# Kernel optimization log

Hardware: AMD Instinct MI355X
Metric: run time of the kernel (lower is better)

The kernel has to match this reference:

```python
import jax, jax.numpy as jnp
import numpy as np

WINDOW = 512
GLOBAL = 64
NEG = -1e9


def setup_inputs() -> dict:
    key = jax.random.key(0)
    kq, kk, kv = jax.random.split(key, 3)
    B, H, S, D = 2, 16, 4096, 64
    q = jax.random.normal(kq, (B, H, S, D), dtype=jnp.float32)
    k = jax.random.normal(kk, (B, H, S, D), dtype=jnp.float32)
    v = jax.random.normal(kv, (B, H, S, D), dtype=jnp.float32)
    return {"q": q, "k": k, "v": v}


def _swa(q, k, v):
    # Causal sliding-window attention (window WINDOW, inclusive of self)
    # with the first GLOBAL queries attending to ALL keys (non-causal),
    # matching the torch reference's per-position SDPA loop.
    B, H, S, D = q.shape
    W, G = WINDOW, GLOBAL
    nb = S // W  # seq chosen as multiple of window
    scale = jnp.asarray(1.0 / np.sqrt(D), q.dtype)

    # --- banded (sliding-window) part, computed blockwise ---
    qb = q.reshape(B, H, nb, W, D)
    # pad one window of zeros in front so each query block sees blocks [b-1, b]
    kp = jnp.pad(k, ((0, 0), (0, 0), (W, 0), (0, 0))).reshape(B, H, nb + 1, W, D)
    vp = jnp.pad(v, ((0, 0), (0, 0), (W, 0), (0, 0))).reshape(B, H, nb + 1, W, D)
    kc = jnp.concatenate([kp[:, :, :nb], kp[:, :, 1:]], axis=3)  # (B,H,nb,2W,D)
    vc = jnp.concatenate([vp[:, :, :nb], vp[:, :, 1:]], axis=3)  # (B,H,nb,2W,D)

    scores = jnp.einsum("bhnqd,bhnkd->bhnqk", qb, kc) * scale  # (B,H,nb,W,2W)

    # query global pos i = b*W + r; key global pos j = (b-1)*W + c, c in [0,2W)
    # window constraint i-W+1 <= j <= i  <=>  r+1 <= c <= r+W
    r = jnp.arange(W)[:, None]
    c = jnp.arange(2 * W)[None, :]
    band = (c >= r + 1) & (c <= r + W)              # (W, 2W)
    first = band & (c >= W)                          # block 0: j >= 0
    blk0 = (jnp.arange(nb) == 0)[:, None, None]
    mask = jnp.where(blk0, first[None], band[None])  # (nb, W, 2W)

    scores = jnp.where(mask[None, None], scores, jnp.asarray(NEG, scores.dtype))
    probs = jax.nn.softmax(scores, axis=-1)
    out = jnp.einsum("bhnqk,bhnkd->bhnqd", probs, vc).reshape(B, H, S, D)

    # --- global prefix: first G queries attend to all keys ---
    sg = jnp.einsum("bhqd,bhkd->bhqk", q[:, :, :G], k) * scale  # (B,H,G,S)
    og = jnp.einsum("bhqk,bhkd->bhqd", jax.nn.softmax(sg, axis=-1), v)
    return out.at[:, :, :G].set(og)


def reference(q, k, v):
    return _swa(q, k, v)
```

## Files before the change

kernel.cpp:

```cpp
#include <hip/hip_runtime.h>


typedef __attribute__((ext_vector_type(4))) float  f32x4;
typedef __attribute__((ext_vector_type(8))) short  s16x8;

#define S_LEN  4096
#define D_HEAD 64
#define SCALE_L2 (0.125f * 1.44269504088896340736f)
#define MINIT  (-1e5f)
#define MASKV  (-1e30f)

static __device__ __forceinline__ short f2bf(float x) {
  unsigned u = __builtin_bit_cast(unsigned, x);
  return (short)((u + 0x8000u) >> 16);
}

static __device__ __forceinline__ f32x4 mfma32(s16x8 a, s16x8 b, f32x4 c) {
  return __builtin_amdgcn_mfma_f32_16x16x32_bf16(a, b, c, 0, 0, 0);
}

extern "C" __global__ void __launch_bounds__(256, 4)
swa_fused_kernel(const float* __restrict__ qg, const float* __restrict__ kg,
                 const float* __restrict__ vg, float* __restrict__ outg) {
  __shared__ __align__(16) char LDSBUF[32768];
  __shared__ float MLB[4][2][16];

  const int tid = threadIdx.x;
  const int w   = tid >> 6;
  const int l   = tid & 63;
  const int g   = l >> 4;
  const int ql  = l & 15;
  const int bi  = blockIdx.x;

  if (bi < 128) {
    const int bh = bi >> 2, qsub = bi & 3;
    const float* Q = qg + (size_t)bh * S_LEN * D_HEAD;
    const float* K = kg + (size_t)bh * S_LEN * D_HEAD;
    const float* V = vg + (size_t)bh * S_LEN * D_HEAD;
    float* O = outg + (size_t)bh * S_LEN * D_HEAD;
    const int qrow = qsub * 16 + ql;

    s16x8 qf[2];
#pragma unroll
    for (int h = 0; h < 2; ++h) {
      const float* p = Q + qrow * 64 + h * 32 + g * 8;
      f32x4 a = *(const f32x4*)p, b = *(const f32x4*)(p + 4);
      s16x8 r;
#pragma unroll
      for (int e = 0; e < 4; ++e) { r[e] = f2bf(a[e] * SCALE_L2); r[4 + e] = f2bf(b[e] * SCALE_L2); }
      qf[h] = r;
    }

    short* kfw = (short*)(LDSBUF + w * 8192);
    short* vfw = (short*)(LDSBUF + w * 8192 + 4096);

    f32x4 acc[4] = {{0,0,0,0},{0,0,0,0},{0,0,0,0},{0,0,0,0}};
    float m = MINIT, lsum = 0.f;

    for (int it = 0; it < 32; ++it) {
      const int k0 = w * 1024 + it * 32;
#pragma unroll
      for (int fb = 0; fb < 4; ++fb) {
        int row = k0 + ((fb >> 1) << 4) + ql;
        int d0  = ((fb & 1) << 5) + (g << 3);
        const float* p = K + row * 64 + d0;
        f32x4 a = *(const f32x4*)p, b = *(const f32x4*)(p + 4);
        s16x8 r;
#pragma unroll
        for (int e = 0; e < 4; ++e) { r[e] = f2bf(a[e]); r[4 + e] = f2bf(b[e]); }
        *(s16x8*)(kfw + (fb * 64 + l) * 8) = r;
      }
#pragma unroll
      for (int fb = 0; fb < 4; ++fb) {
        int dd = fb * 16 + ql;
        int kk = k0 + (g << 2);
        const float* p = V + kk * 64 + dd;
        s16x8 r;
#pragma unroll
        for (int j = 0; j < 4; ++j) { r[j] = f2bf(p[j * 64]); r[4 + j] = f2bf(p[(16 + j) * 64]); }
        *(s16x8*)(vfw + (fb * 64 + l) * 8) = r;
      }
      f32x4 c[2];
#pragma unroll
      for (int kt = 0; kt < 2; ++kt) {
        s16x8 a0 = *(const s16x8*)(kfw + ((kt * 2 + 0) * 64 + l) * 8);
        s16x8 a1 = *(const s16x8*)(kfw + ((kt * 2 + 1) * 64 + l) * 8);
        f32x4 cc = {0,0,0,0};
        cc = mfma32(a0, qf[0], cc);
        cc = mfma32(a1, qf[1], cc);
        c[kt] = cc;
      }
      float rm = MASKV;
#pragma unroll
      for (int kt = 0; kt < 2; ++kt)
#pragma unroll
        for (int r = 0; r < 4; ++r) rm = fmaxf(rm, c[kt][r]);
      rm = fmaxf(rm, __shfl_xor(rm, 16));
      rm = fmaxf(rm, __shfl_xor(rm, 32));
      float mn = fmaxf(m, rm);
      float al = __builtin_amdgcn_exp2f(m - mn);
      float rs = 0.f;
      float pv[2][4];
#pragma unroll
      for (int kt = 0; kt < 2; ++kt)
#pragma unroll
        for (int r = 0; r < 4; ++r) { float e2 = __builtin_amdgcn_exp2f(c[kt][r] - mn); pv[kt][r] = e2; rs += e2; }
      rs += __shfl_xor(rs, 16);
      rs += __shfl_xor(rs, 32);
      lsum = lsum * al + rs;
      m = mn;
#pragma unroll
      for (int dt = 0; dt < 4; ++dt) acc[dt] *= al;
      s16x8 pb;
#pragma unroll
      for (int r = 0; r < 4; ++r) { pb[r] = f2bf(pv[0][r]); pb[4 + r] = f2bf(pv[1][r]); }
#pragma unroll
      for (int dt = 0; dt < 4; ++dt) {
        s16x8 vf = *(const s16x8*)(vfw + (dt * 64 + l) * 8);
        acc[dt] = mfma32(vf, pb, acc[dt]);
      }
    }
    if (g == 0) { MLB[w][0][ql] = m; MLB[w][1][ql] = lsum; }
    __syncthreads();
    {
      float M = fmaxf(fmaxf(MLB[0][0][ql], MLB[1][0][ql]), fmaxf(MLB[2][0][ql], MLB[3][0][ql]));
      float f = __builtin_amdgcn_exp2f(m - M);
      float* mrg = (float*)LDSBUF;
#pragma unroll
      for (int dt = 0; dt < 4; ++dt) {
        f32x4 o = acc[dt] * f;
        *(f32x4*)(mrg + ((w * 4 + dt) * 64 + l) * 4) = o;
      }
    }
    __syncthreads();
    {
      float* mrg = (float*)LDSBUF;
      const int dt = tid >> 6, ln = tid & 63;
      f32x4 s = {0,0,0,0};
#pragma unroll
      for (int ww = 0; ww < 4; ++ww) s += *(const f32x4*)(mrg + ((ww * 4 + dt) * 64 + ln) * 4);
      const int qq = ln & 15;
      float M2 = fmaxf(fmaxf(MLB[0][0][qq], MLB[1][0][qq]), fmaxf(MLB[2][0][qq], MLB[3][0][qq]));
      float L2 = MLB[0][1][qq] * __builtin_amdgcn_exp2f(MLB[0][0][qq] - M2)
               + MLB[1][1][qq] * __builtin_amdgcn_exp2f(MLB[1][0][qq] - M2)
               + MLB[2][1][qq] * __builtin_amdgcn_exp2f(MLB[2][0][qq] - M2)
               + MLB[3][1][qq] * __builtin_amdgcn_exp2f(MLB[3][0][qq] - M2);
      s *= (1.0f / L2);
      *(f32x4*)(O + (size_t)(qsub * 16 + qq) * 64 + dt * 16 + (ln >> 4) * 4) = s;
    }
    return;
  }

  const int idx  = bi - 128;
  const int bh   = idx / 63;
  const int tile = 1 + (idx % 63);
  const float* Q = qg + (size_t)bh * S_LEN * D_HEAD;
  const float* K = kg + (size_t)bh * S_LEN * D_HEAD;
  const float* V = vg + (size_t)bh * S_LEN * D_HEAD;
  float* O = outg + (size_t)bh * S_LEN * D_HEAD;
  const int qrow = tile * 64 + w * 16 + ql;

  s16x8 qf[2];
#pragma unroll
  for (int h = 0; h < 2; ++h) {
    const float* p = Q + qrow * 64 + h * 32 + g * 8;
    f32x4 a = *(const f32x4*)p, b = *(const f32x4*)(p + 4);
    s16x8 r;
#pragma unroll
    for (int e = 0; e < 4; ++e) { r[e] = f2bf(a[e] * SCALE_L2); r[4 + e] = f2bf(b[e] * SCALE_L2); }
    qf[h] = r;
  }

  short* kfrag = (short*)LDSBUF;
  short* vfrag = (short*)(LDSBUF + 16384);

  f32x4 acc[4] = {{0,0,0,0},{0,0,0,0},{0,0,0,0},{0,0,0,0}};
  float m = MINIT, lsum = 0.f;
  const int kb0 = (tile >= 8) ? (tile - 8) : 0;

  for (int kb = kb0; kb <= tile; ++kb) {
    const int k0 = kb * 64;
    __syncthreads();
#pragma unroll
    for (int s2 = 0; s2 < 2; ++s2) {
      int s = tid + s2 * 256;
      int fb = s >> 6, ln = s & 63;
      int row = k0 + ((fb >> 1) << 4) + (ln & 15);
      int d0  = ((fb & 1) << 5) + ((ln >> 4) << 3);
      const float* p = K + row * 64 + d0;
      f32x4 a = *(const f32x4*)p, b = *(const f32x4*)(p + 4);
      s16x8 r;
#pragma unroll
      for (int e = 0; e < 4; ++e) { r[e] = f2bf(a[e]); r[4 + e] = f2bf(b[e]); }
      *(s16x8*)(kfrag + s * 8) = r;
    }
#pragma unroll
    for (int s2 = 0; s2 < 2; ++s2) {
      int s = tid + s2 * 256;
      int fb = s >> 6, ln = s & 63;
      int t = fb >> 2, dt = fb & 3;
      int dd = dt * 16 + (ln & 15);
      int kk = k0 + t * 32 + ((ln >> 4) << 2);
      const float* p = V + kk * 64 + dd;
      s16x8 r;
#pragma unroll
      for (int j = 0; j < 4; ++j) { r[j] = f2bf(p[j * 64]); r[4 + j] = f2bf(p[(16 + j) * 64]); }
      *(s16x8*)(vfrag + s * 8) = r;
    }
    __syncthreads();

    f32x4 c[4];
#pragma unroll
    for (int kt = 0; kt < 4; ++kt) {
      s16x8 a0 = *(const s16x8*)(kfrag + ((kt * 2 + 0) * 64 + l) * 8);
      s16x8 a1 = *(const s16x8*)(kfrag + ((kt * 2 + 1) * 64 + l) * 8);
      f32x4 cc = {0,0,0,0};
      cc = mfma32(a0, qf[0], cc);
      cc = mfma32(a1, qf[1], cc);
      c[kt] = cc;
    }
    if (kb == tile || kb == tile - 8) {
#pragma unroll
      for (int kt = 0; kt < 4; ++kt)
#pragma unroll
        for (int r = 0; r < 4; ++r) {
          int j = k0 + kt * 16 + g * 4 + r;
          bool ok = (j <= qrow) && (j >= qrow - 511);
          c[kt][r] = ok ? c[kt][r] : MASKV;
        }
    }
    float rm = MASKV;
#pragma unroll
    for (int kt = 0; kt < 4; ++kt)
#pragma unroll
      for (int r = 0; r < 4; ++r) rm = fmaxf(rm, c[kt][r]);
    rm = fmaxf(rm, __shfl_xor(rm, 16));
    rm = fmaxf(rm, __shfl_xor(rm, 32));
    float mn = fmaxf(m, rm);
    float al = __builtin_amdgcn_exp2f(m - mn);
    float rs = 0.f;
    float pv[4][4];
#pragma unroll
    for (int kt = 0; kt < 4; ++kt)
#pragma unroll
      for (int r = 0; r < 4; ++r) { float e2 = __builtin_amdgcn_exp2f(c[kt][r] - mn); pv[kt][r] = e2; rs += e2; }
    rs += __shfl_xor(rs, 16);
    rs += __shfl_xor(rs, 32);
    lsum = lsum * al + rs;
    m = mn;
#pragma unroll
    for (int dt = 0; dt < 4; ++dt) acc[dt] *= al;
#pragma unroll
    for (int t = 0; t < 2; ++t) {
      s16x8 pb;
#pragma unroll
      for (int r = 0; r < 4; ++r) { pb[r] = f2bf(pv[2 * t][r]); pb[4 + r] = f2bf(pv[2 * t + 1][r]); }
#pragma unroll
      for (int dt = 0; dt < 4; ++dt) {
        s16x8 vf = *(const s16x8*)(vfrag + ((t * 4 + dt) * 64 + l) * 8);
        acc[dt] = mfma32(vf, pb, acc[dt]);
      }
    }
  }

  const float inv = 1.0f / lsum;
#pragma unroll
  for (int dt = 0; dt < 4; ++dt) {
    f32x4 o = acc[dt] * inv;
    *(f32x4*)(O + (size_t)qrow * 64 + dt * 16 + g * 4) = o;
  }
}

extern "C" void kernel_launch(void* const* d_in, const int* in_sizes, int n_in,
                              void* d_out, int out_size, void* d_ws, size_t ws_size,
                              hipStream_t stream) {
  (void)in_sizes; (void)n_in; (void)d_ws; (void)ws_size; (void)out_size;
  const float* q = (const float*)d_in[0];
  const float* k = (const float*)d_in[1];
  const float* v = (const float*)d_in[2];
  float* o = (float*)d_out;
  dim3 grid(128 + 32 * 63), block(256);
  hipLaunchKernelGGL(swa_fused_kernel, grid, block, 0, stream, q, k, v, o);
}
```

Baseline: 222.8 us.

## Enlarge query tiles to 256 rows with double-buffered K/V staging

The sliding-window blocks now each cover 256 queries (64 per wave) instead of 64, so every converted K/V tile in LDS is reused across four query sub-tiles. K/V loads for the next tile are prefetched into registers and written to a second LDS buffer while the current tile is computed. The global-prefix blocks drop the four-wave split-K merge in favour of one block per head that streams all 64 key tiles with the same double buffer. Grid shrinks to 544 blocks and launch bounds drop to 2 waves per SIMD, trading occupancy and a long serial global-prefix block for much less redundant K/V traffic and bf16 conversion.

```diff
diff --git a/kernel.cpp b/kernel.cpp
--- a/kernel.cpp
+++ b/kernel.cpp
@@ -19,27 +19,74 @@
   return __builtin_amdgcn_mfma_f32_16x16x32_bf16(a, b, c, 0, 0, 0);
 }
 
-extern "C" __global__ void __launch_bounds__(256, 4)
+struct Stage {
+  f32x4 ka[2][2];
+  float vs[2][8];
+};
+
+static __device__ __forceinline__ void stage_load(const float* __restrict__ K,
+                                                  const float* __restrict__ V,
+                                                  int k0, int tid, Stage& st) {
+#pragma unroll
+  for (int i = 0; i < 2; ++i) {
+    int s = tid + i * 256;
+    int fb = s >> 6, ln = s & 63;
+    {
+      int row = k0 + ((fb >> 1) << 4) + (ln & 15);
+      int d0  = ((fb & 1) << 5) + ((ln >> 4) << 3);
+      const float* p = K + row * 64 + d0;
+      st.ka[i][0] = *(const f32x4*)p;
+      st.ka[i][1] = *(const f32x4*)(p + 4);
+    }
+    {
+      int t = fb >> 2, dt = fb & 3;
+      int dd = dt * 16 + (ln & 15);
+      int kk = k0 + t * 32 + ((ln >> 4) << 2);
+      const float* p = V + kk * 64 + dd;
+#pragma unroll
+      for (int j = 0; j < 4; ++j) { st.vs[i][j] = p[j * 64]; st.vs[i][4 + j] = p[(16 + j) * 64]; }
+    }
+  }
+}
+
+static __device__ __forceinline__ void stage_write(short* kf, short* vf, int tid, const Stage& st) {
+#pragma unroll
+  for (int i = 0; i < 2; ++i) {
+    int s = tid + i * 256;
+    s16x8 kr, vr;
+#pragma unroll
+    for (int e = 0; e < 4; ++e) { kr[e] = f2bf(st.ka[i][0][e]); kr[4 + e] = f2bf(st.ka[i][1][e]); }
+#pragma unroll
+    for (int e = 0; e < 8; ++e) vr[e] = f2bf(st.vs[i][e]);
+    *(s16x8*)(kf + s * 8) = kr;
+    *(s16x8*)(vf + s * 8) = vr;
+  }
+}
+
+extern "C" __global__ void __launch_bounds__(256, 2)
 swa_fused_kernel(const float* __restrict__ qg, const float* __restrict__ kg,
                  const float* __restrict__ vg, float* __restrict__ outg) {
-  __shared__ __align__(16) char LDSBUF[32768];
-  __shared__ float MLB[4][2][16];
+  __shared__ __align__(16) short KB[2][4096];
+  __shared__ __align__(16) short VB[2][4096];
 
   const int tid = threadIdx.x;
-  const int w   = tid >> 6;
-  const int l   = tid & 63;
-  const int g   = l >> 4;
-  const int ql  = l & 15;
-  const int bi  = blockIdx.x;
-
-  if (bi < 128) {
-    const int bh = bi >> 2, qsub = bi & 3;
-    const float* Q = qg + (size_t)bh * S_LEN * D_HEAD;
-    const float* K = kg + (size_t)bh * S_LEN * D_HEAD;
-    const float* V = vg + (size_t)bh * S_LEN * D_HEAD;
-    float* O = outg + (size_t)bh * S_LEN * D_HEAD;
-    const int qrow = qsub * 16 + ql;
-
+  const int w  = tid >> 6;
+  const int l  = tid & 63;
+  const int g  = l >> 4;
+  const int ql = l & 15;
+  const int bx = blockIdx.x;
+  const int t  = bx >> 5;
+  const int bh = bx & 31;
+
+  const float* Q = qg + (size_t)bh * S_LEN * D_HEAD;
+  const float* K = kg + (size_t)bh * S_LEN * D_HEAD;
+  const float* V = vg + (size_t)bh * S_LEN * D_HEAD;
+  float* O = outg + (size_t)bh * S_LEN * D_HEAD;
+
+  Stage st;
+
+  if (t == 0) {
+    const int qrow = w * 16 + ql;
     s16x8 qf[2];
 #pragma unroll
     for (int h = 0; h < 2; ++h) {
@@ -50,59 +97,39 @@
       for (int e = 0; e < 4; ++e) { r[e] = f2bf(a[e] * SCALE_L2); r[4 + e] = f2bf(b[e] * SCALE_L2); }
       qf[h] = r;
     }
-
-    short* kfw = (short*)(LDSBUF + w * 8192);
-    short* vfw = (short*)(LDSBUF + w * 8192 + 4096);
-
     f32x4 acc[4] = {{0,0,0,0},{0,0,0,0},{0,0,0,0},{0,0,0,0}};
     float m = MINIT, lsum = 0.f;
 
-    for (int it = 0; it < 32; ++it) {
-      const int k0 = w * 1024 + it * 32;
-#pragma unroll
-      for (int fb = 0; fb < 4; ++fb) {
-        int row = k0 + ((fb >> 1) << 4) + ql;
-        int d0  = ((fb & 1) << 5) + (g << 3);
-        const float* p = K + row * 64 + d0;
-        f32x4 a = *(const f32x4*)p, b = *(const f32x4*)(p + 4);
-        s16x8 r;
-#pragma unroll
-        for (int e = 0; e < 4; ++e) { r[e] = f2bf(a[e]); r[4 + e] = f2bf(b[e]); }
-        *(s16x8*)(kfw + (fb * 64 + l) * 8) = r;
-      }
-#pragma unroll
-      for (int fb = 0; fb < 4; ++fb) {
-        int dd = fb * 16 + ql;
-        int kk = k0 + (g << 2);
-        const float* p = V + kk * 64 + dd;
-        s16x8 r;
-#pragma unroll
-        for (int j = 0; j < 4; ++j) { r[j] = f2bf(p[j * 64]); r[4 + j] = f2bf(p[(16 + j) * 64]); }
-        *(s16x8*)(vfw + (fb * 64 + l) * 8) = r;
-      }
-      f32x4 c[2];
-#pragma unroll
-      for (int kt = 0; kt < 2; ++kt) {
-        s16x8 a0 = *(const s16x8*)(kfw + ((kt * 2 + 0) * 64 + l) * 8);
-        s16x8 a1 = *(const s16x8*)(kfw + ((kt * 2 + 1) * 64 + l) * 8);
-        f32x4 cc = {0,0,0,0};
-        cc = mfma32(a0, qf[0], cc);
-        cc = mfma32(a1, qf[1], cc);
-        c[kt] = cc;
+    stage_load(K, V, 0, tid, st);
+    stage_write(KB[0], VB[0], tid, st);
+    __syncthreads();
+    int cur = 0;
+    for (int kb = 0; kb < 64; ++kb) {
+      if (kb < 63) stage_load(K, V, (kb + 1) * 64, tid, st);
+      const short* kf = KB[cur];
+      const short* vf = VB[cur];
+      f32x4 c[4];
+#pragma unroll
+      for (int kt = 0; kt < 4; ++kt) {
+        s16x8 a0 = *(const s16x8*)(kf + ((kt * 2 + 0) * 64 + l) * 8);
+        s16x8 a1 = *(const s16x8*)(kf + ((kt * 2 + 1) * 64 + l) * 8);
+        f32x4 z = {0,0,0,0};
+        z = mfma32(a0, qf[0], z);
+        c[kt] = mfma32(a1, qf[1], z);
       }
       float rm = MASKV;
 #pragma unroll
-      for (int kt = 0; kt < 2; ++kt)
+      for (int kt = 0; kt < 4; ++kt)
 #pragma unroll
         for (int r = 0; r < 4; ++r) rm = fmaxf(rm, c[kt][r]);
       rm = fmaxf(rm, __shfl_xor(rm, 16));
       rm = fmaxf(rm, __shfl_xor(rm, 32));
       float mn = fmaxf(m, rm);
       float al = __builtin_amdgcn_exp2f(m - mn);
+      float pv[4][4];
       float rs = 0.f;
-      float pv[2][4];
-#pragma unroll
-      for (int kt = 0; kt < 2; ++kt)
+#pragma unroll
+      for (int kt = 0; kt < 4; ++kt)
 #pragma unroll
         for (int r = 0; r < 4; ++r) { float e2 = __builtin_amdgcn_exp2f(c[kt][r] - mn); pv[kt][r] = e2; rs += e2; }
       rs += __shfl_xor(rs, 16);
@@ -111,163 +138,152 @@
       m = mn;
 #pragma unroll
       for (int dt = 0; dt < 4; ++dt) acc[dt] *= al;
-      s16x8 pb;
-#pragma unroll
-      for (int r = 0; r < 4; ++r) { pb[r] = f2bf(pv[0][r]); pb[4 + r] = f2bf(pv[1][r]); }
-#pragma unroll
-      for (int dt = 0; dt < 4; ++dt) {
-        s16x8 vf = *(const s16x8*)(vfw + (dt * 64 + l) * 8);
-        acc[dt] = mfma32(vf, pb, acc[dt]);
-      }
-    }
-    if (g == 0) { MLB[w][0][ql] = m; MLB[w][1][ql] = lsum; }
-    __syncthreads();
-    {
-      float M = fmaxf(fmaxf(MLB[0][0][ql], MLB[1][0][ql]), fmaxf(MLB[2][0][ql], MLB[3][0][ql]));
-      float f = __builtin_amdgcn_exp2f(m - M);
-      float* mrg = (float*)LDSBUF;
-#pragma unroll
-      for (int dt = 0; dt < 4; ++dt) {
-        f32x4 o = acc[dt] * f;
-        *(f32x4*)(mrg + ((w * 4 + dt) * 64 + l) * 4) = o;
-      }
-    }
-    __syncthreads();
-    {
-      float* mrg = (float*)LDSBUF;
-      const int dt = tid >> 6, ln = tid & 63;
-      f32x4 s = {0,0,0,0};
-#pragma unroll
-      for (int ww = 0; ww < 4; ++ww) s += *(const f32x4*)(mrg + ((ww * 4 + dt) * 64 + ln) * 4);
-      const int qq = ln & 15;
-      float M2 = fmaxf(fmaxf(MLB[0][0][qq], MLB[1][0][qq]), fmaxf(MLB[2][0][qq], MLB[3][0][qq]));
-      float L2 = MLB[0][1][qq] * __builtin_amdgcn_exp2f(MLB[0][0][qq] - M2)
-               + MLB[1][1][qq] * __builtin_amdgcn_exp2f(MLB[1][0][qq] - M2)
-               + MLB[2][1][qq] * __builtin_amdgcn_exp2f(MLB[2][0][qq] - M2)
-               + MLB[3][1][qq] * __builtin_amdgcn_exp2f(MLB[3][0][qq] - M2);
-      s *= (1.0f / L2);
-      *(f32x4*)(O + (size_t)(qsub * 16 + qq) * 64 + dt * 16 + (ln >> 4) * 4) = s;
+#pragma unroll
+      for (int tt = 0; tt < 2; ++tt) {
+        s16x8 pb;
+#pragma unroll
+        for (int r = 0; r < 4; ++r) { pb[r] = f2bf(pv[2 * tt][r]); pb[4 + r] = f2bf(pv[2 * tt + 1][r]); }
+#pragma unroll
+        for (int dt = 0; dt < 4; ++dt) {
+          s16x8 vfr = *(const s16x8*)(vf + ((tt * 4 + dt) * 64 + l) * 8);
+          acc[dt] = mfma32(vfr, pb, acc[dt]);
+        }
+      }
+      if (kb < 63) stage_write(KB[cur ^ 1], VB[cur ^ 1], tid, st);
+      __syncthreads();
+      cur ^= 1;
+    }
+    const float inv = 1.0f / lsum;
+#pragma unroll
+    for (int dt = 0; dt < 4; ++dt) {
+      f32x4 o = acc[dt] * inv;
+      *(f32x4*)(O + (size_t)qrow * 64 + dt * 16 + g * 4) = o;
     }
     return;
   }
 
-  const int idx  = bi - 128;
-  const int bh   = idx / 63;
-  const int tile = 1 + (idx % 63);
-  const float* Q = qg + (size_t)bh * S_LEN * D_HEAD;
-  const float* K = kg + (size_t)bh * S_LEN * D_HEAD;
-  const float* V = vg + (size_t)bh * S_LEN * D_HEAD;
-  float* O = outg + (size_t)bh * S_LEN * D_HEAD;
-  const int qrow = tile * 64 + w * 16 + ql;
-
-  s16x8 qf[2];
-#pragma unroll
-  for (int h = 0; h < 2; ++h) {
-    const float* p = Q + qrow * 64 + h * 32 + g * 8;
-    f32x4 a = *(const f32x4*)p, b = *(const f32x4*)(p + 4);
-    s16x8 r;
-#pragma unroll
-    for (int e = 0; e < 4; ++e) { r[e] = f2bf(a[e] * SCALE_L2); r[4 + e] = f2bf(b[e] * SCALE_L2); }
-    qf[h] = r;
-  }
-
-  short* kfrag = (short*)LDSBUF;
-  short* vfrag = (short*)(LDSBUF + 16384);
-
-  f32x4 acc[4] = {{0,0,0,0},{0,0,0,0},{0,0,0,0},{0,0,0,0}};
-  float m = MINIT, lsum = 0.f;
-  const int kb0 = (tile >= 8) ? (tile - 8) : 0;
-
-  for (int kb = kb0; kb <= tile; ++kb) {
-    const int k0 = kb * 64;
-    __syncthreads();
-#pragma unroll
-    for (int s2 = 0; s2 < 2; ++s2) {
-      int s = tid + s2 * 256;
-      int fb = s >> 6, ln = s & 63;
-      int row = k0 + ((fb >> 1) << 4) + (ln & 15);
-      int d0  = ((fb & 1) << 5) + ((ln >> 4) << 3);
-      const float* p = K + row * 64 + d0;
+  const int tb = t - 1;
+  const int Q0 = tb * 256;
+  const int qbase = Q0 + w * 64;
+
+  s16x8 qf[4][2];
+#pragma unroll
+  for (int qt = 0; qt < 4; ++qt)
+#pragma unroll
+    for (int h = 0; h < 2; ++h) {
+      const float* p = Q + (qbase + qt * 16 + ql) * 64 + h * 32 + g * 8;
       f32x4 a = *(const f32x4*)p, b = *(const f32x4*)(p + 4);
       s16x8 r;
 #pragma unroll
-      for (int e = 0; e < 4; ++e) { r[e] = f2bf(a[e]); r[4 + e] = f2bf(b[e]); }
-      *(s16x8*)(kfrag + s * 8) = r;
-    }
-#pragma unroll
-    for (int s2 = 0; s2 < 2; ++s2) {
-      int s = tid + s2 * 256;
-      int fb = s >> 6, ln = s & 63;
-      int t = fb >> 2, dt = fb & 3;
-      int dd = dt * 16 + (ln & 15);
-      int kk = k0 + t * 32 + ((ln >> 4) << 2);
-      const float* p = V + kk * 64 + dd;
-      s16x8 r;
-#pragma unroll
-      for (int j = 0; j < 4; ++j) { r[j] = f2bf(p[j * 64]); r[4 + j] = f2bf(p[(16 + j) * 64]); }
-      *(s16x8*)(vfrag + s * 8) = r;
-    }
+      for (int e = 0; e < 4; ++e) { r[e] = f2bf(a[e] * SCALE_L2); r[4 + e] = f2bf(b[e] * SCALE_L2); }
+      qf[qt][h] = r;
+    }
+
+  f32x4 acc[4][4];
+#pragma unroll
+  for (int qt = 0; qt < 4; ++qt)
+#pragma unroll
+    for (int dt = 0; dt < 4; ++dt) acc[qt][dt] = f32x4{0,0,0,0};
+  float mm[4] = {MINIT, MINIT, MINIT, MINIT};
+  float ll[4] = {0.f, 0.f, 0.f, 0.f};
+
+  const int kbs = (tb >= 2) ? (4 * tb - 8) : 0;
+  const int kbe = 4 * tb + 3;
+
+  stage_load(K, V, kbs * 64, tid, st);
+  stage_write(KB[0], VB[0], tid, st);
+  __syncthreads();
+  int cur = 0;
+  for (int kb = kbs; kb <= kbe; ++kb) {
+    if (kb < kbe) stage_load(K, V, (kb + 1) * 64, tid, st);
+    const short* kf = KB[cur];
+    const short* vf = VB[cur];
+
+    f32x4 c[4][4];
+#pragma unroll
+    for (int kt = 0; kt < 4; ++kt) {
+      s16x8 a0 = *(const s16x8*)(kf + ((kt * 2 + 0) * 64 + l) * 8);
+      s16x8 a1 = *(const s16x8*)(kf + ((kt * 2 + 1) * 64 + l) * 8);
+#pragma unroll
+      for (int qt = 0; qt < 4; ++qt) {
+        f32x4 z = {0,0,0,0};
+        z = mfma32(a0, qf[qt][0], z);
+        c[qt][kt] = mfma32(a1, qf[qt][1], z);
+      }
+    }
+
+    const bool needmask = (kb < 4 * tb - 4) || (kb > 4 * tb - 1);
+
+    s16x8 pbq[4][2];
+#pragma unroll
+    for (int qt = 0; qt < 4; ++qt) {
+      const int qrow = qbase + qt * 16 + ql;
+      if (needmask) {
+#pragma unroll
+        for (int kt = 0; kt < 4; ++kt)
+#pragma unroll
+          for (int r = 0; r < 4; ++r) {
+            int j = kb * 64 + kt * 16 + g * 4 + r;
+            bool ok = (j <= qrow) && (j >= qrow - 511);
+            c[qt][kt][r] = ok ? c[qt][kt][r] : MASKV;
+          }
+      }
+      float rm = MASKV;
+#pragma unroll
+      for (int kt = 0; kt < 4; ++kt)
+#pragma unroll
+        for (int r = 0; r < 4; ++r) rm = fmaxf(rm, c[qt][kt][r]);
+      rm = fmaxf(rm, __shfl_xor(rm, 16));
+      rm = fmaxf(rm, __shfl_xor(rm, 32));
+      float mn = fmaxf(mm[qt], rm);
+      float al = __builtin_amdgcn_exp2f(mm[qt] - mn);
+      float pv[4][4];
+      float rs = 0.f;
+#pragma unroll
+      for (int kt = 0; kt < 4; ++kt)
+#pragma unroll
+        for (int r = 0; r < 4; ++r) { float e2 = __builtin_amdgcn_exp2f(c[qt][kt][r] - mn); pv[kt][r] = e2; rs += e2; }
+      rs += __shfl_xor(rs, 16);
+      rs += __shfl_xor(rs, 32);
+      ll[qt] = ll[qt] * al + rs;
+      mm[qt] = mn;
+#pragma unroll
+      for (int dt = 0; dt < 4; ++dt) acc[qt][dt] *= al;
+#pragma unroll
+      for (int tt = 0; tt < 2; ++tt) {
+        s16x8 pb;
+#pragma unroll
+        for (int r = 0; r < 4; ++r) { pb[r] = f2bf(pv[2 * tt][r]); pb[4 + r] = f2bf(pv[2 * tt + 1][r]); }
+        pbq[qt][tt] = pb;
+      }
+    }
+
+#pragma unroll
+    for (int tt = 0; tt < 2; ++tt)
+#pragma unroll
+      for (int dt = 0; dt < 4; ++dt) {
+        s16x8 vfr = *(const s16x8*)(vf + ((tt * 4 + dt) * 64 + l) * 8);
+#pragma unroll
+        for (int qt = 0; qt < 4; ++qt)
+          acc[qt][dt] = mfma32(vfr, pbq[qt][tt], acc[qt][dt]);
+      }
+
+    if (kb < kbe) stage_write(KB[cur ^ 1], VB[cur ^ 1], tid, st);
     __syncthreads();
-
-    f32x4 c[4];
-#pragma unroll
-    for (int kt = 0; kt < 4; ++kt) {
-      s16x8 a0 = *(const s16x8*)(kfrag + ((kt * 2 + 0) * 64 + l) * 8);
-      s16x8 a1 = *(const s16x8*)(kfrag + ((kt * 2 + 1) * 64 + l) * 8);
-      f32x4 cc = {0,0,0,0};
-      cc = mfma32(a0, qf[0], cc);
-      cc = mfma32(a1, qf[1], cc);
-      c[kt] = cc;
-    }
-    if (kb == tile || kb == tile - 8) {
-#pragma unroll
-      for (int kt = 0; kt < 4; ++kt)
-#pragma unroll
-        for (int r = 0; r < 4; ++r) {
-          int j = k0 + kt * 16 + g * 4 + r;
-          bool ok = (j <= qrow) && (j >= qrow - 511);
-          c[kt][r] = ok ? c[kt][r] : MASKV;
-        }
-    }
-    float rm = MASKV;
-#pragma unroll
-    for (int kt = 0; kt < 4; ++kt)
-#pragma unroll
-      for (int r = 0; r < 4; ++r) rm = fmaxf(rm, c[kt][r]);
-    rm = fmaxf(rm, __shfl_xor(rm, 16));
-    rm = fmaxf(rm, __shfl_xor(rm, 32));
-    float mn = fmaxf(m, rm);
-    float al = __builtin_amdgcn_exp2f(m - mn);
-    float rs = 0.f;
-    float pv[4][4];
-#pragma unroll
-    for (int kt = 0; kt < 4; ++kt)
-#pragma unroll
-      for (int r = 0; r < 4; ++r) { float e2 = __builtin_amdgcn_exp2f(c[kt][r] - mn); pv[kt][r] = e2; rs += e2; }
-    rs += __shfl_xor(rs, 16);
-    rs += __shfl_xor(rs, 32);
-    lsum = lsum * al + rs;
-    m = mn;
-#pragma unroll
-    for (int dt = 0; dt < 4; ++dt) acc[dt] *= al;
-#pragma unroll
-    for (int t = 0; t < 2; ++t) {
-      s16x8 pb;
-#pragma unroll
-      for (int r = 0; r < 4; ++r) { pb[r] = f2bf(pv[2 * t][r]); pb[4 + r] = f2bf(pv[2 * t + 1][r]); }
+    cur ^= 1;
+  }
+
+#pragma unroll
+  for (int qt = 0; qt < 4; ++qt) {
+    if (qbase + qt * 16 >= 64) {
+      const int qrow = qbase + qt * 16 + ql;
+      const float inv = 1.0f / ll[qt];
 #pragma unroll
       for (int dt = 0; dt < 4; ++dt) {
-        s16x8 vf = *(const s16x8*)(vfrag + ((t * 4 + dt) * 64 + l) * 8);
-        acc[dt] = mfma32(vf, pb, acc[dt]);
-      }
-    }
-  }
-
-  const float inv = 1.0f / lsum;
-#pragma unroll
-  for (int dt = 0; dt < 4; ++dt) {
-    f32x4 o = acc[dt] * inv;
-    *(f32x4*)(O + (size_t)qrow * 64 + dt * 16 + g * 4) = o;
+        f32x4 o = acc[qt][dt] * inv;
+        *(f32x4*)(O + (size_t)qrow * 64 + dt * 16 + g * 4) = o;
+      }
+    }
   }
 }
 
@@ -279,6 +295,6 @@
   const float* k = (const float*)d_in[1];
   const float* v = (const float*)d_in[2];
   float* o = (float*)d_out;
-  dim3 grid(128 + 32 * 63), block(256);
+  dim3 grid(17 * 32), block(256);
   hipLaunchKernelGGL(swa_fused_kernel, grid, block, 0, stream, q, k, v, o);
 }
```

Result: faster. 193.4 us (-13.2%).
